# Performance work log

Measured on AMD Instinct MI355X. Metric: run time of the kernel, lower is better.

Reference implementation:

```python
import jax, jax.numpy as jnp
from jax import lax
import numpy as np

B = 2; C = 128; H = 128; W = 128; NPIX = H * W
HTH = 184; HTW = 180; NBINS = HTH * HTW
NSPH = 16384; KHT = 8; KSPH = 16
N0, N1, N2 = 1024, 256, 64
K0, K1, K2 = 8, 8, 8
EPS = 1e-5


def setup_inputs() -> dict:
    key = jax.random.key(0)
    ks = jax.random.split(key, 24)
    f32 = jnp.float32
    inp = {}
    inp["image"] = jax.random.normal(ks[0], (B, C, H, W), f32)
    inp["bn_gamma"] = jnp.ones((C,), f32)
    inp["bn_beta"] = jnp.zeros((C,), f32)
    inp["ht_idx"] = jax.random.randint(ks[1], (NBINS, KHT), 0, NPIX, jnp.int32)
    inp["ht_w"] = jax.random.uniform(ks[2], (NBINS, KHT), f32)
    inp["w_htconv"] = jax.random.normal(ks[3], (3, 3, C, C), f32) / np.sqrt(9.0 * C)
    inp["htbn_gamma"] = jnp.ones((C,), f32)
    inp["htbn_beta"] = jnp.zeros((C,), f32)
    inp["sph_idx"] = jax.random.randint(ks[4], (NSPH, KSPH), 0, NBINS, jnp.int32)
    inp["sph_w"] = jax.random.uniform(ks[5], (NSPH, KSPH), f32)
    inp["w_sc"] = jax.random.normal(ks[6], (3, 64, C), f32) / np.sqrt(1.0 * C)
    inp["b_sc"] = jnp.zeros((3, 64), f32)
    inp["scbn_gamma"] = jnp.ones((3, 64), f32)
    inp["scbn_beta"] = jnp.zeros((3, 64), f32)
    inp["dgcn_w"] = jax.random.normal(ks[7], (3, 4, 128, 64), f32) / np.sqrt(128.0)
    inp["dgcn_b"] = jnp.zeros((3, 4, 64), f32)
    inp["dgcn_hw"] = jax.random.normal(ks[8], (3, 64), f32) / 8.0
    inp["dgcn_hb"] = jnp.zeros((3,), f32)
    inp["ind0"] = jax.random.randint(ks[9], (B, N0), 0, NSPH, jnp.int32)
    inp["ind1"] = jax.random.randint(ks[10], (B, 3, N1), 0, NSPH, jnp.int32)
    inp["ind2"] = jax.random.randint(ks[11], (B, 3, N2), 0, NSPH, jnp.int32)
    # kNN-style edges: structured centers (each node repeated k times), random neighbors
    c0 = jnp.tile(jnp.repeat(jnp.arange(N0, dtype=jnp.int32), K0)[None], (B, 1))
    inp["edge0"] = jnp.stack([c0, jax.random.randint(ks[12], (B, N0 * K0), 0, N0, jnp.int32)], 1)
    c1 = jnp.broadcast_to(jnp.repeat(jnp.arange(N1, dtype=jnp.int32), K1)[None, None], (B, 3, N1 * K1))
    inp["edge1"] = jnp.stack([c1, jax.random.randint(ks[13], (B, 3, N1 * K1), 0, N1, jnp.int32)], 2)
    c2 = jnp.broadcast_to(jnp.repeat(jnp.arange(N2, dtype=jnp.int32), K2)[None, None], (B, 3, N2 * K2))
    inp["edge2"] = jnp.stack([c2, jax.random.randint(ks[14], (B, 3, N2 * K2), 0, N2, jnp.int32)], 2)
    inp["target0"] = jax.random.randint(ks[15], (B, N0), 0, 2, jnp.int32)
    inp["target1"] = jax.random.randint(ks[16], (B * 3, N1), 0, 2, jnp.int32)
    inp["target2"] = jax.random.randint(ks[17], (B * 3, N2), 0, 2, jnp.int32)
    return inp


def _bn2d(x, g, b):
    m = x.mean((0, 2, 3), keepdims=True)
    v = x.var((0, 2, 3), keepdims=True)
    return g[None, :, None, None] * (x - m) * lax.rsqrt(v + EPS) + b[None, :, None, None]


def _sphere(x_htf, sph_idx, sph_w, ind):
    # x_htf: [B,C,NBINS]; ind: [B,S] -> weighted gather of HT bins per sphere node
    mi = sph_idx[ind]          # [B,S,K]
    mw = sph_w[ind]            # [B,S,K]
    g = jax.vmap(lambda xb, ib: xb[:, ib])(x_htf, mi)   # [B,C,S,K]
    return (g * mw[:, None]).sum(-1)                    # [B,C,S]


def _sconv(x, w, b, g, be):
    # 1x1 conv [B,C,S]->[B,64,S] + BN1d (batch stats) + ReLU
    y = jnp.einsum('oc,bcs->bos', w, x) + b[None, :, None]
    m = y.mean((0, 2), keepdims=True)
    v = y.var((0, 2), keepdims=True)
    return jax.nn.relu(g[None, :, None] * (y - m) * lax.rsqrt(v + EPS) + be[None, :, None])


def _dgcn(x, edge, ws, bs, hw, hb, n, k):
    # x: [Bg,n,64]; edge: [Bg,2,n*k] (row0=center, row1=neighbor); 4 EdgeConv layers
    for i in range(4):
        xc = jnp.take_along_axis(x, edge[:, 0, :, None], axis=1)   # [Bg,n*k,Cin]
        xn = jnp.take_along_axis(x, edge[:, 1, :, None], axis=1)
        h = jax.nn.relu(jnp.concatenate([xc, xn - xc], -1) @ ws[i] + bs[i])
        x = h.reshape(x.shape[0], n, k, -1).max(2)                 # max over neighbors
    return x @ hw + hb                                             # [Bg,n] logits


def _bce(logits, target):
    t = target.astype(logits.dtype)
    l = jnp.maximum(logits, 0.0) - logits * t + jnp.log1p(jnp.exp(-jnp.abs(logits)))
    pos = t > 0.5
    npos = jnp.maximum(pos.sum(), 1).astype(l.dtype)
    nneg = jnp.maximum((~pos).sum(), 1).astype(l.dtype)
    return jnp.where(pos, l, 0.0).sum() / npos, jnp.where(pos, 0.0, l).sum() / nneg


def _forward(image, bn_gamma, bn_beta, ht_idx, ht_w, w_htconv, htbn_gamma, htbn_beta,
             sph_idx, sph_w, w_sc, b_sc, scbn_gamma, scbn_beta,
             dgcn_w, dgcn_b, dgcn_hw, dgcn_hb,
             ind0, ind1, ind2, edge0, edge1, edge2, target0, target1, target2):
    x = jax.nn.relu(_bn2d(image, bn_gamma, bn_beta))
    xf = x.reshape(B, C, NPIX)
    # Hough voting: each HT bin accumulates KHT weighted pixels
    ht = (xf[:, :, ht_idx] * ht_w).sum(-1).reshape(B, C, HTH, HTW)
    hc = lax.conv_general_dilated(ht, w_htconv, (1, 1), 'SAME',
                                  dimension_numbers=('NCHW', 'HWIO', 'NCHW'))
    x_htf = jax.nn.relu(_bn2d(hc, htbn_gamma, htbn_beta)).reshape(B, C, NBINS)

    # scale 0
    x0 = _sconv(_sphere(x_htf, sph_idx, sph_w, ind0),
                w_sc[0], b_sc[0], scbn_gamma[0], scbn_beta[0]).transpose(0, 2, 1)
    x0 = _dgcn(x0, edge0, dgcn_w[0], dgcn_b[0], dgcn_hw[0], dgcn_hb[0], N0, K0)   # [B,N0]
    # scale 1 (3 vanishing-point branches folded into batch)
    x1 = _sconv(_sphere(x_htf, sph_idx, sph_w, ind1.reshape(B, -1)),
                w_sc[1], b_sc[1], scbn_gamma[1], scbn_beta[1]).transpose(0, 2, 1)
    x1 = _dgcn(x1.reshape(B * 3, N1, 64), edge1.reshape(B * 3, 2, N1 * K1),
               dgcn_w[1], dgcn_b[1], dgcn_hw[1], dgcn_hb[1], N1, K1)              # [B*3,N1]
    # scale 2
    x2 = _sconv(_sphere(x_htf, sph_idx, sph_w, ind2.reshape(B, -1)),
                w_sc[2], b_sc[2], scbn_gamma[2], scbn_beta[2]).transpose(0, 2, 1)
    x2 = _dgcn(x2.reshape(B * 3, N2, 64), edge2.reshape(B * 3, 2, N2 * K2),
               dgcn_w[2], dgcn_b[2], dgcn_hw[2], dgcn_hb[2], N2, K2)              # [B*3,N2]

    lp0, ln0 = _bce(x0, target0)
    lp1, ln1 = _bce(x1, target1)
    lp2, ln2 = _bce(x2, target2)
    losses = jnp.stack([lp0, ln0, lp1, ln1, lp2, ln2])
    preds = jnp.concatenate([jax.nn.sigmoid(x0).reshape(B, -1),
                             jax.nn.sigmoid(x1).reshape(B, -1),
                             jax.nn.sigmoid(x2).reshape(B, -1)], axis=1)
    return losses, preds


def reference(image, bn_gamma, bn_beta, ht_idx, ht_w, w_htconv, htbn_gamma, htbn_beta,
              sph_idx, sph_w, w_sc, b_sc, scbn_gamma, scbn_beta,
              dgcn_w, dgcn_b, dgcn_hw, dgcn_hb,
              ind0, ind1, ind2, edge0, edge1, edge2, target0, target1, target2):
    return _forward(image, bn_gamma, bn_beta, ht_idx, ht_w, w_htconv, htbn_gamma, htbn_beta,
                    sph_idx, sph_w, w_sc, b_sc, scbn_gamma, scbn_beta,
                    dgcn_w, dgcn_b, dgcn_hw, dgcn_hb,
                    ind0, ind1, ind2, edge0, edge1, edge2, target0, target1, target2)
```

## Files before the change

### kernel.cpp

```cpp
#include <hip/hip_runtime.h>
#include <math.h>

#define B_ 2
#define C_ 128
#define NPIX_ 16384
#define HTH_ 184
#define HTW_ 180
#define NBINS_ 33120
#define PH_ 186
#define PW_ 184
#define NPB_ 1984
#define TOTN_ 3968
#define EPS_ 1e-5f

#define ST_HC_SUM 0
#define ST_HC_SQ  128
#define ST_SC_SUM 256
#define ST_SC_SQ  448
#define ST_LOSS   640
#define ST_TICKET 652
#define ST_IMG_S1 1472
#define ST_IMG_S2 1600

typedef __attribute__((ext_vector_type(8))) short v8s;
typedef __attribute__((ext_vector_type(4))) float v4f;

__device__ inline unsigned short f2b(float f) {
  unsigned u = __builtin_bit_cast(unsigned, f);
  unsigned r = u + 0x7fffu + ((u >> 16) & 1u);
  return (unsigned short)(r >> 16);
}
__device__ inline float b2f(unsigned short u) {
  unsigned v = ((unsigned)u) << 16;
  return __builtin_bit_cast(float, v);
}

__global__ void kprep0(const float* __restrict__ w, const float* __restrict__ dw,
                       const float* __restrict__ wsc,
                       unsigned short* __restrict__ wtb, unsigned short* __restrict__ dwb,
                       unsigned short* __restrict__ swb,
                       unsigned* __restrict__ htb2, const float* __restrict__ img,
                       float* __restrict__ st) {
  int bid = blockIdx.x;
  int tid = threadIdx.x;
  if (bid < 1612) {
    int idx = bid*256 + tid;
    if (idx < 147456) {
      int tap = idx >> 14, z = idx & 16383;
      int j = z & 7, lane = (z >> 3) & 63, nt = (z >> 9) & 7, kt = (z >> 12) & 3;
      int l = lane & 15, q = lane >> 4;
      int co = nt*16 + l, ci = kt*32 + q*8 + j;
      wtb[idx] = f2b(w[(tap*C_ + ci)*C_ + co]);
    } else if (idx < 245760) {
      int i2 = idx - 147456;
      int sl = i2 >> 13, z = i2 & 8191;
      int j = z & 7, lane = (z >> 3) & 63, nt = (z >> 9) & 3, kt = (z >> 11) & 3;
      int l = lane & 15, q = lane >> 4;
      int co = nt*16 + l, cc = kt*32 + q*8 + j;
      dwb[i2] = f2b(dw[(sl*128 + cc)*64 + co]);
    } else if (idx < 270336) {
      int i3 = idx - 245760;
      int s = i3 >> 13, z = i3 & 8191;
      int j = z & 7, lane = (z >> 3) & 63, nt = (z >> 9) & 3, kt = (z >> 11) & 3;
      int l = lane & 15, q = lane >> 4;
      int co = nt*16 + l, cc = kt*32 + q*8 + j;
      swb[i3] = f2b(wsc[(s*64 + co)*128 + cc]);
    } else if (idx < 412672) {
      int i = idx - 270336;
      int d = i & 63;
      int cell = i >> 6;
      int b = cell / 1112, j = cell % 1112;
      int y, x;
      if (j < 184) { y = 0; x = j; }
      else if (j < 368) { y = 185; x = j - 184; }
      else { int c = j - 368; int xi = c / 186; y = c % 186; x = xi == 0 ? 0 : 180 + xi; }
      htb2[((size_t)(b*PH_ + y)*PW_ + x)*64 + d] = 0u;
    }
  } else {
    int kb = bid - 1612;
    int c = kb >> 3, chunk = kb & 7;
    float s1 = 0.f, s2 = 0.f;
    for (int i = chunk*4096 + tid; i < (chunk+1)*4096; i += 256) {
      int b = i >> 14, p = i & (NPIX_-1);
      float v = img[((size_t)(b*C_ + c))*NPIX_ + p];
      s1 += v; s2 += v*v;
    }
    __shared__ float r1[256], r2[256];
    r1[tid] = s1; r2[tid] = s2; __syncthreads();
    for (int off = 128; off; off >>= 1) {
      if (tid < off) { r1[tid] += r1[tid+off]; r2[tid] += r2[tid+off]; }
      __syncthreads();
    }
    if (tid == 0) {
      atomicAdd(&st[ST_IMG_S1 + c], r1[0]);
      atomicAdd(&st[ST_IMG_S2 + c], r2[0]);
    }
  }
}

__global__ void k2_bnrelu_t(const float* __restrict__ img, const float* __restrict__ st,
                            const float* __restrict__ g, const float* __restrict__ be,
                            unsigned short* __restrict__ xt) {
  __shared__ float tile[32*65];
  __shared__ float ash[32], dsh[32];
  int p0 = blockIdx.x*64, c0 = blockIdx.y*32, b = blockIdx.z;
  int tid = threadIdx.x;
  if (tid < 32) {
    int c = c0 + tid;
    float n = (float)(B_*NPIX_);
    float m = st[ST_IMG_S1+c]/n;
    float var = st[ST_IMG_S2+c]/n - m*m;
    float a = g[c]*rsqrtf(var + EPS_);
    ash[tid] = a; dsh[tid] = be[c] - a*m;
  }
  __syncthreads();
  for (int r = 0; r < 8; r++) {
    int flat = tid + r*256;
    int row = flat >> 6, col = flat & 63;
    float v = img[((size_t)(b*C_ + c0 + row))*NPIX_ + p0 + col];
    tile[row*65 + col] = fmaxf(ash[row]*v + dsh[row], 0.f);
  }
  __syncthreads();
  for (int r = 0; r < 4; r++) {
    int flat = (tid + r*256)*2;
    int pl = flat >> 5, cl = flat & 31;
    unsigned lo = f2b(tile[cl*65 + pl]);
    unsigned hi = f2b(tile[(cl+1)*65 + pl]);
    *(unsigned*)&xt[((size_t)b*NPIX_ + p0 + pl)*C_ + c0 + cl] = lo | (hi << 16);
  }
}

__global__ void k3_hough(const unsigned* __restrict__ xt2, const int* __restrict__ hidx,
                         const float* __restrict__ hwt, unsigned* __restrict__ htb2) {
  int tid = threadIdx.x;
  int wv = __builtin_amdgcn_readfirstlane(tid >> 6);
  int lane = tid & 63;
  int b = blockIdx.y;
  int bin0 = blockIdx.x*16 + wv*4;
  const unsigned* base = xt2 + (size_t)b*NPIX_*64 + lane;
  unsigned dv[4][8];
  #pragma unroll
  for (int i = 0; i < 4; i++) {
    #pragma unroll
    for (int k = 0; k < 8; k++) {
      int p = hidx[(bin0+i)*8 + k];
      dv[i][k] = base[(size_t)p*64];
    }
  }
  #pragma unroll
  for (int i = 0; i < 4; i++) {
    int bin = bin0 + i;
    float acc0 = 0.f, acc1 = 0.f;
    #pragma unroll
    for (int k = 0; k < 8; k++) {
      float w = hwt[bin*8 + k];
      acc0 += w * b2f((unsigned short)(dv[i][k] & 0xffff));
      acc1 += w * b2f((unsigned short)(dv[i][k] >> 16));
    }
    int y = bin / HTW_, x = bin - y*HTW_;
    htb2[((size_t)(b*PH_ + y + 1)*PW_ + (x+1))*64 + lane] =
        (unsigned)f2b(acc0) | (((unsigned)f2b(acc1)) << 16);
  }
}

__global__ __launch_bounds__(256, 3) void k4_mfma(
    const unsigned short* __restrict__ htb, const unsigned short* __restrict__ wtb,
    unsigned short* __restrict__ hcb, float* __restrict__ st) {
  __shared__ char smem[32768];
  int tid = threadIdx.x;
  int wav = tid >> 6, lane = tid & 63;
  int quad = lane >> 4, l16 = lane & 15;
  int b = blockIdx.y;
  int p0 = blockIdx.x*128 + wav*32;
  size_t ab[2];
  #pragma unroll
  for (int t = 0; t < 2; t++) {
    int px = p0 + t*16 + l16; if (px > NBINS_-1) px = NBINS_-1;
    int y = px / HTW_, x = px % HTW_;
    ab[t] = (((size_t)(b*PH_ + y))*PW_ + x)*C_ + quad*8;
  }
  v4f acc[2][8];
  #pragma unroll
  for (int t = 0; t < 2; t++)
    #pragma unroll
    for (int nt = 0; nt < 8; nt++) acc[t][nt] = (v4f){0,0,0,0};

  for (int tap = 0; tap < 9; tap++) {
    __syncthreads();
    const uint4* src = (const uint4*)(wtb + tap*16384);
    uint4* dst = (uint4*)smem;
    #pragma unroll
    for (int s = 0; s < 8; s++) dst[tid + s*256] = src[tid + s*256];
    __syncthreads();
    int dy = tap/3, dx = tap - dy*3;
    int toff = (dy*PW_ + dx)*C_;
    v8s a[2][4];
    #pragma unroll
    for (int t = 0; t < 2; t++)
      #pragma unroll
      for (int kt = 0; kt < 4; kt++)
        a[t][kt] = *(const v8s*)&htb[ab[t] + toff + kt*32];
    #pragma unroll
    for (int kt = 0; kt < 4; kt++) {
      #pragma unroll
      for (int nt = 0; nt < 8; nt++) {
        v8s bf = *(const v8s*)(smem + ((((kt*8 + nt)*64) + lane) << 4));
        acc[0][nt] = __builtin_amdgcn_mfma_f32_16x16x32_bf16(a[0][kt], bf, acc[0][nt], 0, 0, 0);
        acc[1][nt] = __builtin_amdgcn_mfma_f32_16x16x32_bf16(a[1][kt], bf, acc[1][nt], 0, 0, 0);
      }
    }
  }
  __syncthreads();
  float* red = (float*)smem;
  float s1[8], s2[8];
  #pragma unroll
  for (int nt = 0; nt < 8; nt++) { s1[nt] = 0.f; s2[nt] = 0.f; }
  #pragma unroll
  for (int t = 0; t < 2; t++) {
    int pbase = p0 + t*16 + quad*4;
    #pragma unroll
    for (int nt = 0; nt < 8; nt++) {
      int co = nt*16 + l16;
      #pragma unroll
      for (int reg = 0; reg < 4; reg++) {
        int po = pbase + reg;
        if (po < NBINS_) {
          float v = acc[t][nt][reg];
          hcb[((size_t)b*NBINS_ + po)*C_ + co] = f2b(v);
          s1[nt] += v; s2[nt] += v*v;
        }
      }
    }
  }
  int slot = wav*4 + quad;
  #pragma unroll
  for (int nt = 0; nt < 8; nt++) red[(nt*16 + l16)*17 + slot] = s1[nt];
  __syncthreads();
  if (tid < 128) {
    float s = 0.f;
    #pragma unroll
    for (int k = 0; k < 16; k++) s += red[tid*17 + k];
    atomicAdd(&st[ST_HC_SUM + tid], s);
  }
  __syncthreads();
  #pragma unroll
  for (int nt = 0; nt < 8; nt++) red[(nt*16 + l16)*17 + slot] = s2[nt];
  __syncthreads();
  if (tid < 128) {
    float s = 0.f;
    #pragma unroll
    for (int k = 0; k < 16; k++) s += red[tid*17 + k];
    atomicAdd(&st[ST_HC_SQ + tid], s);
  }
}

__global__ __launch_bounds__(256) void k67_sphconv(
    const unsigned* __restrict__ hcb2, const float* __restrict__ g, const float* __restrict__ be,
    const int* __restrict__ sph_idx, const float* __restrict__ sph_w,
    const int* __restrict__ ind0, const int* __restrict__ ind1, const int* __restrict__ ind2,
    const unsigned short* __restrict__ swb, const float* __restrict__ b_sc,
    float* __restrict__ y, float* __restrict__ st) {
  __shared__ unsigned short E[16*136];
  int tid = threadIdx.x;
  int gn0 = blockIdx.x*8;
  int nb0 = gn0 % NPB_;
  int s = nb0 < 1024 ? 0 : (nb0 < 1792 ? 1 : 2);
  int wv = tid >> 6, lane = tid & 63;
  int quad = lane >> 4, l16 = lane & 15;
  {
    int c0 = lane*2, c1 = c0 + 1;
    float n = (float)(B_*NBINS_);
    float m0 = st[ST_HC_SUM + c0]/n, m1 = st[ST_HC_SUM + c1]/n;
    float va0 = st[ST_HC_SQ + c0]/n - m0*m0, va1 = st[ST_HC_SQ + c1]/n - m1*m1;
    float a0 = g[c0]*rsqrtf(va0 + EPS_), a1 = g[c1]*rsqrtf(va1 + EPS_);
    float d0 = be[c0] - a0*m0, d1 = be[c1] - a1*m1;
    #pragma unroll
    for (int i = 0; i < 2; i++) {
      int node_l = wv*2 + i;
      int gn = gn0 + node_l;
      int b = gn / NPB_, nb = gn % NPB_;
      int v;
      if (nb < 1024) v = ind0[b*1024 + nb];
      else if (nb < 1792) v = ind1[b*768 + nb - 1024];
      else v = ind2[b*192 + nb - 1792];
      v = __builtin_amdgcn_readfirstlane(v);
      const unsigned* base = hcb2 + (size_t)b*NBINS_*64 + lane;
      float acc0 = 0.f, acc1 = 0.f;
      #pragma unroll
      for (int k = 0; k < 16; k++) {
        int mi = sph_idx[v*16 + k];
        float mw = sph_w[v*16 + k];
        unsigned dv = base[(size_t)mi*64];
        acc0 += mw * fmaxf(a0*b2f((unsigned short)(dv & 0xffff)) + d0, 0.f);
        acc1 += mw * fmaxf(a1*b2f((unsigned short)(dv >> 16)) + d1, 0.f);
      }
      unsigned lo = f2b(acc0), hi = f2b(acc1);
      *(unsigned*)&E[node_l*136 + c0] = lo | (hi << 16);
    }
  }
  __syncthreads();
  v4f acc = (v4f){0,0,0,0};
  const unsigned short* wb = swb + s*8192 + wv*512;
  #pragma unroll
  for (int kt = 0; kt < 4; kt++) {
    v8s a = *(const v8s*)&E[l16*136 + quad*8 + kt*32];
    v8s bf = *(const v8s*)&wb[kt*2048 + lane*8];
    acc = __builtin_amdgcn_mfma_f32_16x16x32_bf16(a, bf, acc, 0, 0, 0);
  }
  float bias = b_sc[s*64 + wv*16 + l16];
  float s1 = 0.f, s2 = 0.f;
  #pragma unroll
  for (int reg = 0; reg < 4; reg++) {
    int row = quad*4 + reg;
    if (quad < 2) {
      float val = acc[reg] + bias;
      y[(size_t)(gn0 + row)*64 + wv*16 + l16] = val;
      s1 += val; s2 += val*val;
    }
  }
  s1 += __shfl_xor(s1, 16);
  s2 += __shfl_xor(s2, 16);
  if (quad == 0) {
    atomicAdd(&st[ST_SC_SUM + s*64 + wv*16 + l16], s1);
    atomicAdd(&st[ST_SC_SQ  + s*64 + wv*16 + l16], s2);
  }
}

__global__ __launch_bounds__(256) void k10_dgcn(
    const void* __restrict__ xin_, unsigned short* __restrict__ xout,
    const int* __restrict__ edge0, const int* __restrict__ edge1, const int* __restrict__ edge2,
    const unsigned short* __restrict__ dwb, const float* __restrict__ db,
    const float* __restrict__ st, const float* __restrict__ scg, const float* __restrict__ scb,
    int layer, int usebn) {
  __shared__ unsigned short E[64*136];
  __shared__ float ash[64], dsh[64];
  int tid = threadIdx.x;
  int bid = blockIdx.x;
  int s, node_base, le_blk, span; const int* ec;
  if (bid < 256) {
    s = 0; int b = bid >> 7; node_base = b*NPB_; le_blk = (bid & 127)*64;
    span = 8192; ec = edge0 + b*2*8192;
  } else if (bid < 448) {
    int j = bid - 256; s = 1; int seg = j >> 5; int b = seg/3, vp = seg%3;
    node_base = b*NPB_ + 1024 + vp*256; le_blk = (j & 31)*64;
    span = 2048; ec = edge1 + ((b*3+vp)*2)*2048;
  } else {
    int j = bid - 448; s = 2; int seg = j >> 3; int b = seg/3, vp = seg%3;
    node_base = b*NPB_ + 1792 + vp*64; le_blk = (j & 7)*64;
    span = 512; ec = edge2 + ((b*3+vp)*2)*512;
  }
  const int* en = ec + span;
  if (usebn) {
    if (tid < 64) {
      float n = s==0 ? 2048.f : (s==1 ? 1536.f : 384.f);
      float m = st[ST_SC_SUM + s*64 + tid]/n;
      float var = st[ST_SC_SQ + s*64 + tid]/n - m*m;
      float a = scg[s*64 + tid]*rsqrtf(var + EPS_);
      ash[tid] = a; dsh[tid] = scb[s*64 + tid] - a*m;
    }
    __syncthreads();
  }
  {
    int e_l = tid >> 2, part = tid & 3;
    int h = part >> 1, cb = (part & 1)*32;
    int e = le_blk + e_l;
    int ci = ec[e], ni = en[e];
    if (usebn) {
      const float* xc = (const float*)xin_ + (size_t)(node_base + ci)*64 + cb;
      const float* xn = (const float*)xin_ + (size_t)(node_base + ni)*64 + cb;
      float4 xc4[8], xn4[8];
      #pragma unroll
      for (int q = 0; q < 8; q++) xc4[q] = *(const float4*)&xc[q*4];
      if (h) {
        #pragma unroll
        for (int q = 0; q < 8; q++) xn4[q] = *(const float4*)&xn[q*4];
      }
      #pragma unroll
      for (int c8 = 0; c8 < 32; c8 += 8) {
        v8s pk;
        #pragma unroll
        for (int j = 0; j < 8; j++) {
          int cl = c8 + j;
          int c = cb + cl;
          float xcv = ((const float*)xc4)[cl];
          float vc = fmaxf(ash[c]*xcv + dsh[c], 0.f);
          float val = vc;
          if (h) {
            float xnv = ((const float*)xn4)[cl];
            val = fmaxf(ash[c]*xnv + dsh[c], 0.f) - vc;
          }
          pk[j] = (short)f2b(val);
        }
        *(v8s*)&E[e_l*136 + h*64 + cb + c8] = pk;
      }
    } else {
      const unsigned short* xc = (const unsigned short*)xin_ + (size_t)(node_base + ci)*64 + cb;
      const unsigned short* xn = (const unsigned short*)xin_ + (size_t)(node_base + ni)*64 + cb;
      #pragma unroll
      for (int c8 = 0; c8 < 32; c8 += 8) {
        v8s vc8 = *(const v8s*)&xc[c8];
        v8s pk = vc8;
        if (h) {
          v8s vn8 = *(const v8s*)&xn[c8];
          #pragma unroll
          for (int j = 0; j < 8; j++)
            pk[j] = (short)f2b(b2f((unsigned short)vn8[j]) - b2f((unsigned short)vc8[j]));
        }
        *(v8s*)&E[e_l*136 + h*64 + cb + c8] = pk;
      }
    }
  }
  __syncthreads();
  int wave = tid >> 6, lane = tid & 63;
  int quad = lane >> 4, l16 = lane & 15;
  const unsigned short* wb = dwb + (size_t)(s*4 + layer)*8192;
  v4f acc[4];
  #pragma unroll
  for (int nt = 0; nt < 4; nt++) acc[nt] = (v4f){0,0,0,0};
  #pragma unroll
  for (int kt = 0; kt < 4; kt++) {
    v8s a = *(const v8s*)&E[(wave*16 + l16)*136 + quad*8 + kt*32];
    #pragma unroll
    for (int nt = 0; nt < 4; nt++) {
      v8s bf = *(const v8s*)&wb[((kt*4 + nt)*64 + lane)*8];
      acc[nt] = __builtin_amdgcn_mfma_f32_16x16x32_bf16(a, bf, acc[nt], 0, 0, 0);
    }
  }
  #pragma unroll
  for (int nt = 0; nt < 4; nt++) {
    float bias = db[(s*4 + layer)*64 + nt*16 + l16];
    float m = fmaxf(fmaxf(acc[nt][0], acc[nt][1]), fmaxf(acc[nt][2], acc[nt][3]));
    m = fmaxf(m + bias, 0.f);
    float other = __shfl_xor(m, 16);
    m = fmaxf(m, other);
    if ((quad & 1) == 0) {
      int node_l = wave*2 + (quad >> 1);
      xout[(size_t)(node_base + (le_blk >> 3) + node_l)*64 + nt*16 + l16] = f2b(m);
    }
  }
}

__global__ __launch_bounds__(256) void k11_head(
    const unsigned short* __restrict__ x, const float* __restrict__ hw, const float* __restrict__ hb,
    const int* __restrict__ t0, const int* __restrict__ t1, const int* __restrict__ t2,
    float* __restrict__ out, float* __restrict__ st) {
  __shared__ float shw[192];
  int tid = threadIdx.x;
  if (tid < 192) shw[tid] = hw[tid];
  __syncthreads();
  int gn = blockIdx.x*256 + tid;
  bool valid = gn < TOTN_;
  int g = valid ? gn : TOTN_-1;
  int b = g / NPB_, nb = g % NPB_;
  int s, tg;
  if (nb < 1024) { s = 0; tg = t0[b*1024 + nb]; }
  else if (nb < 1792) { s = 1; int j = nb-1024; tg = t1[(b*3 + (j>>8))*256 + (j&255)]; }
  else { s = 2; int j = nb-1792; tg = t2[(b*3 + (j>>6))*64 + (j&63)]; }
  const unsigned short* row = x + (size_t)g*64;
  float logit = hb[s];
  #pragma unroll
  for (int c8 = 0; c8 < 64; c8 += 8) {
    v8s v = *(const v8s*)&row[c8];
    #pragma unroll
    for (int j = 0; j < 8; j++)
      logit += b2f((unsigned short)v[j]) * shw[s*64 + c8 + j];
  }
  if (valid) out[6 + gn] = 1.f / (1.f + expf(-logit));
  float tf = (float)tg;
  float l = fmaxf(logit, 0.f) - logit*tf + log1pf(expf(-fabsf(logit)));
  float sp = (valid && tg) ? l : 0.f;
  float sn = (valid && !tg) ? l : 0.f;
  float cp = (valid && tg) ? 1.f : 0.f;
  float cn = (valid && !tg) ? 1.f : 0.f;
  for (int off = 32; off; off >>= 1) {
    sp += __shfl_down(sp, off);
    sn += __shfl_down(sn, off);
    cp += __shfl_down(cp, off);
    cn += __shfl_down(cn, off);
  }
  if ((tid & 63) == 0) {
    atomicAdd(&st[ST_LOSS + s*4 + 0], sp);
    atomicAdd(&st[ST_LOSS + s*4 + 1], sn);
    atomicAdd(&st[ST_LOSS + s*4 + 2], cp);
    atomicAdd(&st[ST_LOSS + s*4 + 3], cn);
  }
  __syncthreads();
  __threadfence();
  if (tid == 0) {
    unsigned t = (unsigned)atomicAdd(&st[ST_TICKET], 1.f);
    if (t >= 15) {
      #pragma unroll
      for (int i = 0; i < 6; i++) {
        int sc = i >> 1; int pos = !(i & 1);
        float sum = atomicAdd(&st[ST_LOSS + sc*4 + (pos ? 0 : 1)], 0.f);
        float cnt = atomicAdd(&st[ST_LOSS + sc*4 + (pos ? 2 : 3)], 0.f);
        out[i] = sum / fmaxf(cnt, 1.f);
      }
    }
  }
}

extern "C" void kernel_launch(void* const* d_in, const int* in_sizes, int n_in,
                              void* d_out, int out_size, void* d_ws, size_t ws_size,
                              hipStream_t stream) {
  const float* image  = (const float*)d_in[0];
  const float* bn_g   = (const float*)d_in[1];
  const float* bn_b   = (const float*)d_in[2];
  const int*   ht_idx = (const int*)  d_in[3];
  const float* ht_w   = (const float*)d_in[4];
  const float* w_conv = (const float*)d_in[5];
  const float* htbn_g = (const float*)d_in[6];
  const float* htbn_b = (const float*)d_in[7];
  const int*   sph_idx= (const int*)  d_in[8];
  const float* sph_w  = (const float*)d_in[9];
  const float* w_sc   = (const float*)d_in[10];
  const float* b_sc   = (const float*)d_in[11];
  const float* scbn_g = (const float*)d_in[12];
  const float* scbn_b = (const float*)d_in[13];
  const float* dgcn_w = (const float*)d_in[14];
  const float* dgcn_b = (const float*)d_in[15];
  const float* dgcn_hw= (const float*)d_in[16];
  const float* dgcn_hb= (const float*)d_in[17];
  const int*   ind0   = (const int*)  d_in[18];
  const int*   ind1   = (const int*)  d_in[19];
  const int*   ind2   = (const int*)  d_in[20];
  const int*   edge0  = (const int*)  d_in[21];
  const int*   edge1  = (const int*)  d_in[22];
  const int*   edge2  = (const int*)  d_in[23];
  const int*   t0     = (const int*)  d_in[24];
  const int*   t1     = (const int*)  d_in[25];
  const int*   t2     = (const int*)  d_in[26];
  float* out = (float*)d_out;

  char* ws = (char*)d_ws;
  unsigned short* x_t   = (unsigned short*)(ws);
  unsigned short* htb   = (unsigned short*)(ws +  8388608);
  unsigned short* hcb   = (unsigned short*)(ws + 25911296);
  unsigned short* wtb   = (unsigned short*)(ws + 42868736);
  unsigned short* dwb   = (unsigned short*)(ws + 43163648);
  unsigned short* swb   = (unsigned short*)(ws + 43360256);
  float*          y_sc  = (float*)(ws + 43409408);
  unsigned short* xdgA  = (unsigned short*)(ws + 44425216);
  unsigned short* xdgB  = (unsigned short*)(ws + 44933120);
  float*          st    = (float*)(ws + 45441024);

  hipMemsetAsync(st, 0, 1728*sizeof(float), stream);
  kprep0<<<2636, 256, 0, stream>>>(w_conv, dgcn_w, w_sc, wtb, dwb, swb, (unsigned*)htb, image, st);
  k2_bnrelu_t<<<dim3(256,4,2), 256, 0, stream>>>(image, st, bn_g, bn_b, x_t);
  k3_hough<<<dim3(NBINS_/16, B_), 256, 0, stream>>>((const unsigned*)x_t, ht_idx, ht_w, (unsigned*)htb);
  k4_mfma<<<dim3(259, 2), 256, 0, stream>>>(htb, wtb, hcb, st);
  k67_sphconv<<<TOTN_/8, 256, 0, stream>>>((const unsigned*)hcb, htbn_g, htbn_b, sph_idx, sph_w,
                                           ind0, ind1, ind2, swb, b_sc, y_sc, st);
  k10_dgcn<<<496, 256, 0, stream>>>((const void*)y_sc, xdgA, edge0, edge1, edge2, dwb, dgcn_b, st, scbn_g, scbn_b, 0, 1);
  k10_dgcn<<<496, 256, 0, stream>>>((const void*)xdgA, xdgB, edge0, edge1, edge2, dwb, dgcn_b, st, scbn_g, scbn_b, 1, 0);
  k10_dgcn<<<496, 256, 0, stream>>>((const void*)xdgB, xdgA, edge0, edge1, edge2, dwb, dgcn_b, st, scbn_g, scbn_b, 2, 0);
  k10_dgcn<<<496, 256, 0, stream>>>((const void*)xdgA, xdgB, edge0, edge1, edge2, dwb, dgcn_b, st, scbn_g, scbn_b, 3, 0);
  k11_head<<<16, 256, 0, stream>>>(xdgB, dgcn_hw, dgcn_hb, t0, t1, t2, out, st);
}
```

Measured before the change: 239.3 us.

## Split conv output channels across waves and drop memset via partial image stats

The 3x3 MFMA conv kernel now gives each wave half of the output channels for 32 pixels. Blocks cover 64 pixels instead of 128, so the grid doubles, per-wave accumulators shrink, and launch bounds rise to allow 4 blocks per CU. Separately, the image BN statistics are written as per-chunk partials and summed in the consumer, which removes the atomics. An extra block in the prep kernel zeroes the stats buffer, replacing the hipMemsetAsync call. The trade-off is that each weight tile in LDS is now reused across fewer pixels and every A fragment is loaded by two waves.

Result: slower. 257.1 us (+7.5%).

```diff
diff --git a/kernel.cpp b/kernel.cpp
--- a/kernel.cpp
+++ b/kernel.cpp
@@ -19,8 +19,8 @@
 #define ST_SC_SQ  448
 #define ST_LOSS   640
 #define ST_TICKET 652
-#define ST_IMG_S1 1472
-#define ST_IMG_S2 1600
+#define ST_IMG_P1 704
+#define ST_IMG_P2 1728
 
 typedef __attribute__((ext_vector_type(8))) short v8s;
 typedef __attribute__((ext_vector_type(4))) float v4f;
@@ -76,7 +76,7 @@
       else { int c = j - 368; int xi = c / 186; y = c % 186; x = xi == 0 ? 0 : 180 + xi; }
       htb2[((size_t)(b*PH_ + y)*PW_ + x)*64 + d] = 0u;
     }
-  } else {
+  } else if (bid < 2636) {
     int kb = bid - 1612;
     int c = kb >> 3, chunk = kb & 7;
     float s1 = 0.f, s2 = 0.f;
@@ -92,9 +92,11 @@
       __syncthreads();
     }
     if (tid == 0) {
-      atomicAdd(&st[ST_IMG_S1 + c], r1[0]);
-      atomicAdd(&st[ST_IMG_S2 + c], r2[0]);
-    }
+      st[ST_IMG_P1 + chunk*128 + c] = r1[0];
+      st[ST_IMG_P2 + chunk*128 + c] = r2[0];
+    }
+  } else {
+    for (int i = tid; i < 672; i += 256) st[i] = 0.f;
   }
 }
 
@@ -107,9 +109,15 @@
   int tid = threadIdx.x;
   if (tid < 32) {
     int c = c0 + tid;
+    float s1 = 0.f, s2 = 0.f;
+    #pragma unroll
+    for (int ch = 0; ch < 8; ch++) {
+      s1 += st[ST_IMG_P1 + ch*128 + c];
+      s2 += st[ST_IMG_P2 + ch*128 + c];
+    }
     float n = (float)(B_*NPIX_);
-    float m = st[ST_IMG_S1+c]/n;
-    float var = st[ST_IMG_S2+c]/n - m*m;
+    float m = s1/n;
+    float var = s2/n - m*m;
     float a = g[c]*rsqrtf(var + EPS_);
     ash[tid] = a; dsh[tid] = be[c] - a*m;
   }
@@ -163,15 +171,16 @@
   }
 }
 
-__global__ __launch_bounds__(256, 3) void k4_mfma(
+__global__ __launch_bounds__(256, 4) void k4_mfma(
     const unsigned short* __restrict__ htb, const unsigned short* __restrict__ wtb,
     unsigned short* __restrict__ hcb, float* __restrict__ st) {
   __shared__ char smem[32768];
   int tid = threadIdx.x;
   int wav = tid >> 6, lane = tid & 63;
   int quad = lane >> 4, l16 = lane & 15;
+  int ph = wav & 1, ch = wav >> 1;
   int b = blockIdx.y;
-  int p0 = blockIdx.x*128 + wav*32;
+  int p0 = blockIdx.x*64 + ph*32;
   size_t ab[2];
   #pragma unroll
   for (int t = 0; t < 2; t++) {
@@ -179,11 +188,11 @@
     int y = px / HTW_, x = px % HTW_;
     ab[t] = (((size_t)(b*PH_ + y))*PW_ + x)*C_ + quad*8;
   }
-  v4f acc[2][8];
+  v4f acc[2][4];
   #pragma unroll
   for (int t = 0; t < 2; t++)
     #pragma unroll
-    for (int nt = 0; nt < 8; nt++) acc[t][nt] = (v4f){0,0,0,0};
+    for (int nt = 0; nt < 4; nt++) acc[t][nt] = (v4f){0,0,0,0};
 
   for (int tap = 0; tap < 9; tap++) {
     __syncthreads();
@@ -203,8 +212,8 @@
     #pragma unroll
     for (int kt = 0; kt < 4; kt++) {
       #pragma unroll
-      for (int nt = 0; nt < 8; nt++) {
-        v8s bf = *(const v8s*)(smem + ((((kt*8 + nt)*64) + lane) << 4));
+      for (int nt = 0; nt < 4; nt++) {
+        v8s bf = *(const v8s*)(smem + ((((kt*8 + ch*4 + nt)*64) + lane) << 4));
         acc[0][nt] = __builtin_amdgcn_mfma_f32_16x16x32_bf16(a[0][kt], bf, acc[0][nt], 0, 0, 0);
         acc[1][nt] = __builtin_amdgcn_mfma_f32_16x16x32_bf16(a[1][kt], bf, acc[1][nt], 0, 0, 0);
       }
@@ -212,15 +221,13 @@
   }
   __syncthreads();
   float* red = (float*)smem;
-  float s1[8], s2[8];
-  #pragma unroll
-  for (int nt = 0; nt < 8; nt++) { s1[nt] = 0.f; s2[nt] = 0.f; }
+  float s1[4] = {0,0,0,0}, s2[4] = {0,0,0,0};
   #pragma unroll
   for (int t = 0; t < 2; t++) {
     int pbase = p0 + t*16 + quad*4;
     #pragma unroll
-    for (int nt = 0; nt < 8; nt++) {
-      int co = nt*16 + l16;
+    for (int nt = 0; nt < 4; nt++) {
+      int co = ch*64 + nt*16 + l16;
       #pragma unroll
       for (int reg = 0; reg < 4; reg++) {
         int po = pbase + reg;
@@ -232,24 +239,24 @@
       }
     }
   }
-  int slot = wav*4 + quad;
-  #pragma unroll
-  for (int nt = 0; nt < 8; nt++) red[(nt*16 + l16)*17 + slot] = s1[nt];
+  int slot = ph*4 + quad;
+  #pragma unroll
+  for (int nt = 0; nt < 4; nt++) red[(ch*64 + nt*16 + l16)*9 + slot] = s1[nt];
   __syncthreads();
   if (tid < 128) {
     float s = 0.f;
     #pragma unroll
-    for (int k = 0; k < 16; k++) s += red[tid*17 + k];
+    for (int k = 0; k < 8; k++) s += red[tid*9 + k];
     atomicAdd(&st[ST_HC_SUM + tid], s);
   }
   __syncthreads();
   #pragma unroll
-  for (int nt = 0; nt < 8; nt++) red[(nt*16 + l16)*17 + slot] = s2[nt];
+  for (int nt = 0; nt < 4; nt++) red[(ch*64 + nt*16 + l16)*9 + slot] = s2[nt];
   __syncthreads();
   if (tid < 128) {
     float s = 0.f;
     #pragma unroll
-    for (int k = 0; k < 16; k++) s += red[tid*17 + k];
+    for (int k = 0; k < 8; k++) s += red[tid*9 + k];
     atomicAdd(&st[ST_HC_SQ + tid], s);
   }
 }
@@ -544,11 +551,10 @@
   unsigned short* xdgB  = (unsigned short*)(ws + 44933120);
   float*          st    = (float*)(ws + 45441024);
 
-  hipMemsetAsync(st, 0, 1728*sizeof(float), stream);
-  kprep0<<<2636, 256, 0, stream>>>(w_conv, dgcn_w, w_sc, wtb, dwb, swb, (unsigned*)htb, image, st);
+  kprep0<<<2637, 256, 0, stream>>>(w_conv, dgcn_w, w_sc, wtb, dwb, swb, (unsigned*)htb, image, st);
   k2_bnrelu_t<<<dim3(256,4,2), 256, 0, stream>>>(image, st, bn_g, bn_b, x_t);
   k3_hough<<<dim3(NBINS_/16, B_), 256, 0, stream>>>((const unsigned*)x_t, ht_idx, ht_w, (unsigned*)htb);
-  k4_mfma<<<dim3(259, 2), 256, 0, stream>>>(htb, wtb, hcb, st);
+  k4_mfma<<<dim3(518, 2), 256, 0, stream>>>(htb, wtb, hcb, st);
   k67_sphconv<<<TOTN_/8, 256, 0, stream>>>((const unsigned*)hcb, htbn_g, htbn_b, sph_idx, sph_w,
                                            ind0, ind1, ind2, swb, b_sc, y_sc, st);
   k10_dgcn<<<496, 256, 0, stream>>>((const void*)y_sc, xdgA, edge0, edge1, edge2, dwb, dgcn_b, st, scbn_g, scbn_b, 0, 1);
```

## Software-pipeline conv tap loads and replace memset/atomics with partial sums

Applied to the files above, without the earlier changes.

The conv kernel now prefetches the next tap's weights and activation fragments into registers while the MFMAs for the current tap run, then stores the weights to shared memory between barriers. Its launch bounds drop from 3 to 2 blocks per CU so the extra registers fit. The image BN statistics are written as per-chunk partials, which k2 sums, instead of being accumulated with atomics. This lets the hipMemset be removed, with an extra block in kprep0 zeroing the remaining stats. The cost is higher register pressure and lower occupancy in the conv kernel.

After: 276.7 us. +15.7%, slower.

```diff
diff --git a/kernel.cpp b/kernel.cpp
--- a/kernel.cpp
+++ b/kernel.cpp
@@ -19,8 +19,8 @@
 #define ST_SC_SQ  448
 #define ST_LOSS   640
 #define ST_TICKET 652
-#define ST_IMG_S1 1472
-#define ST_IMG_S2 1600
+#define ST_IMG_P1 704
+#define ST_IMG_P2 1728
 
 typedef __attribute__((ext_vector_type(8))) short v8s;
 typedef __attribute__((ext_vector_type(4))) float v4f;
@@ -76,7 +76,7 @@
       else { int c = j - 368; int xi = c / 186; y = c % 186; x = xi == 0 ? 0 : 180 + xi; }
       htb2[((size_t)(b*PH_ + y)*PW_ + x)*64 + d] = 0u;
     }
-  } else {
+  } else if (bid < 2636) {
     int kb = bid - 1612;
     int c = kb >> 3, chunk = kb & 7;
     float s1 = 0.f, s2 = 0.f;
@@ -92,9 +92,11 @@
       __syncthreads();
     }
     if (tid == 0) {
-      atomicAdd(&st[ST_IMG_S1 + c], r1[0]);
-      atomicAdd(&st[ST_IMG_S2 + c], r2[0]);
-    }
+      st[ST_IMG_P1 + chunk*128 + c] = r1[0];
+      st[ST_IMG_P2 + chunk*128 + c] = r2[0];
+    }
+  } else {
+    for (int i = tid; i < 672; i += 256) st[i] = 0.f;
   }
 }
 
@@ -107,9 +109,15 @@
   int tid = threadIdx.x;
   if (tid < 32) {
     int c = c0 + tid;
+    float s1 = 0.f, s2 = 0.f;
+    #pragma unroll
+    for (int ch = 0; ch < 8; ch++) {
+      s1 += st[ST_IMG_P1 + ch*128 + c];
+      s2 += st[ST_IMG_P2 + ch*128 + c];
+    }
     float n = (float)(B_*NPIX_);
-    float m = st[ST_IMG_S1+c]/n;
-    float var = st[ST_IMG_S2+c]/n - m*m;
+    float m = s1/n;
+    float var = s2/n - m*m;
     float a = g[c]*rsqrtf(var + EPS_);
     ash[tid] = a; dsh[tid] = be[c] - a*m;
   }
@@ -163,7 +171,7 @@
   }
 }
 
-__global__ __launch_bounds__(256, 3) void k4_mfma(
+__global__ __launch_bounds__(256, 2) void k4_mfma(
     const unsigned short* __restrict__ htb, const unsigned short* __restrict__ wtb,
     unsigned short* __restrict__ hcb, float* __restrict__ st) {
   __shared__ char smem[32768];
@@ -185,32 +193,57 @@
     #pragma unroll
     for (int nt = 0; nt < 8; nt++) acc[t][nt] = (v4f){0,0,0,0};
 
+  {
+    const uint4* src = (const uint4*)wtb;
+    uint4* dst = (uint4*)smem;
+    #pragma unroll
+    for (int s = 0; s < 8; s++) dst[tid + s*256] = src[tid + s*256];
+  }
+  v8s aCur[2][4];
+  #pragma unroll
+  for (int t = 0; t < 2; t++)
+    #pragma unroll
+    for (int kt = 0; kt < 4; kt++)
+      aCur[t][kt] = *(const v8s*)&htb[ab[t] + kt*32];
+  __syncthreads();
+
   for (int tap = 0; tap < 9; tap++) {
-    __syncthreads();
-    const uint4* src = (const uint4*)(wtb + tap*16384);
-    uint4* dst = (uint4*)smem;
-    #pragma unroll
-    for (int s = 0; s < 8; s++) dst[tid + s*256] = src[tid + s*256];
-    __syncthreads();
-    int dy = tap/3, dx = tap - dy*3;
-    int toff = (dy*PW_ + dx)*C_;
-    v8s a[2][4];
-    #pragma unroll
-    for (int t = 0; t < 2; t++)
-      #pragma unroll
-      for (int kt = 0; kt < 4; kt++)
-        a[t][kt] = *(const v8s*)&htb[ab[t] + toff + kt*32];
+    uint4 wreg[8];
+    v8s aNext[2][4];
+    if (tap < 8) {
+      const uint4* src = (const uint4*)(wtb + (tap+1)*16384);
+      #pragma unroll
+      for (int s = 0; s < 8; s++) wreg[s] = src[tid + s*256];
+      int dy = (tap+1)/3, dx = (tap+1) - dy*3;
+      int toff = (dy*PW_ + dx)*C_;
+      #pragma unroll
+      for (int t = 0; t < 2; t++)
+        #pragma unroll
+        for (int kt = 0; kt < 4; kt++)
+          aNext[t][kt] = *(const v8s*)&htb[ab[t] + toff + kt*32];
+    }
     #pragma unroll
     for (int kt = 0; kt < 4; kt++) {
       #pragma unroll
       for (int nt = 0; nt < 8; nt++) {
         v8s bf = *(const v8s*)(smem + ((((kt*8 + nt)*64) + lane) << 4));
-        acc[0][nt] = __builtin_amdgcn_mfma_f32_16x16x32_bf16(a[0][kt], bf, acc[0][nt], 0, 0, 0);
-        acc[1][nt] = __builtin_amdgcn_mfma_f32_16x16x32_bf16(a[1][kt], bf, acc[1][nt], 0, 0, 0);
-      }
-    }
-  }
-  __syncthreads();
+        acc[0][nt] = __builtin_amdgcn_mfma_f32_16x16x32_bf16(aCur[0][kt], bf, acc[0][nt], 0, 0, 0);
+        acc[1][nt] = __builtin_amdgcn_mfma_f32_16x16x32_bf16(aCur[1][kt], bf, acc[1][nt], 0, 0, 0);
+      }
+    }
+    __syncthreads();
+    if (tap < 8) {
+      uint4* dst = (uint4*)smem;
+      #pragma unroll
+      for (int s = 0; s < 8; s++) dst[tid + s*256] = wreg[s];
+      #pragma unroll
+      for (int t = 0; t < 2; t++)
+        #pragma unroll
+        for (int kt = 0; kt < 4; kt++)
+          aCur[t][kt] = aNext[t][kt];
+    }
+    __syncthreads();
+  }
   float* red = (float*)smem;
   float s1[8], s2[8];
   #pragma unroll
@@ -544,8 +577,7 @@
   unsigned short* xdgB  = (unsigned short*)(ws + 44933120);
   float*          st    = (float*)(ws + 45441024);
 
-  hipMemsetAsync(st, 0, 1728*sizeof(float), stream);
-  kprep0<<<2636, 256, 0, stream>>>(w_conv, dgcn_w, w_sc, wtb, dwb, swb, (unsigned*)htb, image, st);
+  kprep0<<<2637, 256, 0, stream>>>(w_conv, dgcn_w, w_sc, wtb, dwb, swb, (unsigned*)htb, image, st);
   k2_bnrelu_t<<<dim3(256,4,2), 256, 0, stream>>>(image, st, bn_g, bn_b, x_t);
   k3_hough<<<dim3(NBINS_/16, B_), 256, 0, stream>>>((const unsigned*)x_t, ht_idx, ht_w, (unsigned*)htb);
   k4_mfma<<<dim3(259, 2), 256, 0, stream>>>(htb, wtb, hcb, st);
```
